# Kernel optimization log

Hardware: AMD Instinct MI355X
Metric: run time of the kernel (lower is better)

Reference implementation:

```python
import jax, jax.numpy as jnp
import numpy as np

N, E = 4096, 32768
NI, EI, D, EH = 64, 16, 64, 128
NUM_STEPS = 3


def setup_inputs() -> dict:
    key = jax.random.key(0)
    ks = jax.random.split(key, 24)

    def w(k, shape, fan_in):
        return (jax.random.normal(k, shape, jnp.float32) / np.float32(np.sqrt(fan_in)))

    return {
        "node_feats": jax.random.normal(ks[0], (N, NI), jnp.float32),
        "edge_attr": jax.random.normal(ks[1], (E, EI), jnp.float32),
        "edge_index": jax.random.randint(ks[2], (2, E), 0, N),
        # project_node_feats: Linear(NI -> D)
        "W_p": w(ks[3], (NI, D), NI), "b_p": jnp.zeros((D,), jnp.float32),
        # project_edge_feats: Linear(EI -> EH)
        "W_pe": w(ks[4], (EI, EH), EI), "b_pe": jnp.zeros((EH,), jnp.float32),
        # edge_network (NNConv nn): Linear(EH -> D*D)
        "W_nn": w(ks[5], (EH, D * D), EH), "b_nn": jnp.zeros((D * D,), jnp.float32),
        # NNConv root weight + bias
        "W_root": w(ks[6], (D, D), D), "b_conv": jnp.zeros((D,), jnp.float32),
        # GRU (single layer), gate order r, z, n as in torch
        "w_ih": w(ks[7], (D, 3 * D), D), "w_hh": w(ks[8], (D, 3 * D), D),
        "b_ih": jnp.zeros((3 * D,), jnp.float32), "b_hh": jnp.zeros((3 * D,), jnp.float32),
        # edge_update_network: Linear(EH+2D -> EH), Linear(EH -> EH)
        "W_eu1": w(ks[9], (EH + 2 * D, EH), EH + 2 * D), "b_eu1": jnp.zeros((EH,), jnp.float32),
        "W_eu2": w(ks[10], (EH, EH), EH), "b_eu2": jnp.zeros((EH,), jnp.float32),
    }


def reference(node_feats, edge_attr, edge_index, W_p, b_p, W_pe, b_pe,
              W_nn, b_nn, W_root, b_conv, w_ih, w_hh, b_ih, b_hh,
              W_eu1, b_eu1, W_eu2, b_eu2):
    relu = jax.nn.relu
    row, col = edge_index[0], edge_index[1]  # source, target
    n_nodes = node_feats.shape[0]
    d = W_root.shape[0]

    h = relu(node_feats @ W_p + b_p)          # (N, D) projected node feats
    hidden = h                                  # GRU hidden state
    e = relu(edge_attr @ W_pe + b_pe)          # (E, EH) projected edge feats

    for _ in range(NUM_STEPS):
        # NNConv: per-edge weight matrix from edge MLP (dropout=0 in eval)
        We = relu(e @ W_nn + b_nn).reshape(-1, d, d)      # (E, D, D)
        msg = jnp.einsum('ed,edf->ef', h[row], We)        # gather + per-edge matmul
        agg = jax.ops.segment_sum(msg, col, num_segments=n_nodes)  # scatter-add
        m = relu(agg + h @ W_root + b_conv)                # conv output + activation

        # GRU cell (torch gate order: r, z, n)
        gi = m @ w_ih + b_ih
        gh = hidden @ w_hh + b_hh
        ir, iz, i_n = jnp.split(gi, 3, axis=-1)
        hr, hz, h_n = jnp.split(gh, 3, axis=-1)
        r = jax.nn.sigmoid(ir + hr)
        z = jax.nn.sigmoid(iz + hz)
        ncand = jnp.tanh(i_n + r * h_n)
        hidden = (1.0 - z) * ncand + z * hidden
        h = hidden

        # edge update: cat(h[row], h[col], e) -> 2-layer MLP
        ei = jnp.concatenate([h[row], h[col], e], axis=1)
        e = relu(relu(ei @ W_eu1 + b_eu1) @ W_eu2 + b_eu2)

    return h, e
```

## Files before the change

### kernel.cpp

```cpp
#include <hip/hip_runtime.h>
#include <stdint.h>

typedef __attribute__((ext_vector_type(8))) _Float16 f16x8;
typedef __attribute__((ext_vector_type(4))) float f32x4;

#define N_NODES 4096
#define N_EDGES 32768

__device__ __forceinline__ float sigm(float x) { return 1.f / (1.f + __expf(-x)); }

__device__ __forceinline__ f16x8 packh8(const float* p) {
  f16x8 r;
#pragma unroll
  for (int i = 0; i < 8; ++i) r[i] = (_Float16)p[i];
  return r;
}

__device__ __forceinline__ void pinv(f16x8& x) { asm volatile("" : "+v"(x)); }

__global__ void zero_agg_kernel(float* __restrict__ agg) {
  agg[blockIdx.x * 256 + threadIdx.x] = 0.f;
}

__global__ void prep_all(const float* __restrict__ Wnn,
                         const float* __restrict__ We1,
                         const float* __restrict__ We2,
                         _Float16* __restrict__ WnnT,
                         _Float16* __restrict__ We1T,
                         _Float16* __restrict__ We2T) {
  __shared__ float tile[128][33];
  const int b = blockIdx.x, t = threadIdx.x;
  if (b < 128) {
    const int nb = b * 32;
    for (int i = 0; i < 16; ++i) {
      int g = i * 256 + t;
      int k = g >> 5, j = g & 31;
      tile[k][j] = Wnn[(size_t)k * 4096 + nb + j];
    }
    __syncthreads();
    for (int i = 0; i < 16; ++i) {
      int g = i * 256 + t;
      int j = g >> 7, k = g & 127;
      WnnT[(size_t)(nb + j) * 128 + k] = (_Float16)tile[k][j];
    }
  } else {
    int idx = (b - 128) * 256 + t;
    if (idx < 32768) {
      int n = idx >> 8, k = idx & 255;
      We1T[idx] = (_Float16)We1[(size_t)k * 128 + n];
    } else {
      int j = idx - 32768;
      int n = j >> 7, k = j & 127;
      We2T[j] = (_Float16)We2[(size_t)k * 128 + n];
    }
  }
}

__global__ void proj_node_f(const float* __restrict__ nf,
                            const float* __restrict__ Wp,
                            const float* __restrict__ bp,
                            float* __restrict__ h) {
  int idx = blockIdx.x * 256 + threadIdx.x;
  int n = idx >> 6, c = idx & 63;
  float acc = bp[c];
  for (int k = 0; k < 64; ++k)
    acc = fmaf(nf[n * 64 + k], Wp[k * 64 + c], acc);
  h[idx] = fmaxf(acc, 0.f);
}

__launch_bounds__(256)
__global__ void proj_edge_f2(const float* __restrict__ ea,
                             const float* __restrict__ Wpe,
                             const float* __restrict__ bpe,
                             float* __restrict__ e) {
  __shared__ float sw[16 * 128];
  __shared__ float sb[128];
  __shared__ float sa[32][17];
  const int t = threadIdx.x;
  const int ebase = blockIdx.x * 32;
  for (int g = t; g < 2048; g += 256) sw[g] = Wpe[g];
  if (t < 128) sb[t] = bpe[t];
  for (int g = t; g < 512; g += 256) {
    int r = g >> 4, k = g & 15;
    sa[r][k] = ea[(size_t)(ebase + r) * 16 + k];
  }
  __syncthreads();
  int c = t & 127, eg = t >> 7;
  float wc[16];
#pragma unroll
  for (int k = 0; k < 16; ++k) wc[k] = sw[k * 128 + c];
  float bv = sb[c];
#pragma unroll
  for (int i = 0; i < 16; ++i) {
    int ee = eg * 16 + i;
    float acc = bv;
#pragma unroll
    for (int k = 0; k < 16; ++k) acc = fmaf(sa[ee][k], wc[k], acc);
    e[(size_t)(ebase + ee) * 128 + c] = fmaxf(acc, 0.f);
  }
}

__launch_bounds__(512, 1)
__global__ void fused_msg_m(const float* __restrict__ ebf,
                            const float* __restrict__ hid,
                            const _Float16* __restrict__ WnnT,
                            const float* __restrict__ bnn,
                            const int* __restrict__ eidx,
                            float* __restrict__ agg) {
  __shared__ float Hs[64 * 132];
  const int t = threadIdx.x;
  const int w = t >> 6, l = t & 63, l15 = l & 15, q = l >> 4;
  const int fw = w & 3;
  const int eh = w >> 2;
  const int ebase = blockIdx.x * 128;

#pragma unroll
  for (int i = 0; i < 4; ++i) {
    int g = i * 512 + t;
    int e = g >> 4, d4 = g & 15;
    int r = eidx[ebase + e];
    float4 v = *(const float4*)&hid[(size_t)r * 64 + d4 * 4];
    Hs[(d4 * 4 + 0) * 132 + e] = v.x;
    Hs[(d4 * 4 + 1) * 132 + e] = v.y;
    Hs[(d4 * 4 + 2) * 132 + e] = v.z;
    Hs[(d4 * 4 + 3) * 132 + e] = v.w;
  }

  f16x8 af[4][4];
#pragma unroll
  for (int m = 0; m < 4; ++m)
#pragma unroll
    for (int kk = 0; kk < 4; ++kk) {
      af[m][kk] = packh8(&ebf[(size_t)(ebase + eh * 64 + m * 16 + l15) * 128 + kk * 32 + q * 8]);
      pinv(af[m][kk]);
    }

  float msg[4][4];
#pragma unroll
  for (int m = 0; m < 4; ++m)
#pragma unroll
    for (int rr = 0; rr < 4; ++rr) msg[m][rr] = 0.f;

  __syncthreads();

  const _Float16* wb = WnnT + (size_t)(fw * 16 + l15) * 128 + q * 8;
  f16x8 bb[4], nb[4];
#pragma unroll
  for (int kk = 0; kk < 4; ++kk) bb[kk] = *(const f16x8*)(wb + kk * 32);

  for (int d = 0; d < 64; ++d) {
    if (d < 63) {
      const _Float16* p = wb + (size_t)(d + 1) * 8192;
#pragma unroll
      for (int kk = 0; kk < 4; ++kk) nb[kk] = *(const f16x8*)(p + kk * 32);
    }
    float bnv = bnn[d * 64 + fw * 16 + l15];
#pragma unroll
    for (int m = 0; m < 4; ++m) {
      f32x4 C = {0.f, 0.f, 0.f, 0.f};
#pragma unroll
      for (int kk = 0; kk < 4; ++kk)
        C = __builtin_amdgcn_mfma_f32_16x16x32_f16(af[m][kk], bb[kk], C, 0, 0, 0);
      float4 hv = *(const float4*)&Hs[d * 132 + eh * 64 + m * 16 + q * 4];
      msg[m][0] = fmaf(hv.x, fmaxf(C[0] + bnv, 0.f), msg[m][0]);
      msg[m][1] = fmaf(hv.y, fmaxf(C[1] + bnv, 0.f), msg[m][1]);
      msg[m][2] = fmaf(hv.z, fmaxf(C[2] + bnv, 0.f), msg[m][2]);
      msg[m][3] = fmaf(hv.w, fmaxf(C[3] + bnv, 0.f), msg[m][3]);
    }
#pragma unroll
    for (int kk = 0; kk < 4; ++kk) bb[kk] = nb[kk];
  }

  const int* colp = eidx + N_EDGES;
#pragma unroll
  for (int m = 0; m < 4; ++m)
#pragma unroll
    for (int rr = 0; rr < 4; ++rr) {
      int col = colp[ebase + eh * 64 + m * 16 + q * 4 + rr];
      atomicAdd(&agg[(size_t)col * 64 + fw * 16 + l15], msg[m][rr]);
    }
}

__global__ void node_update_f(const float* __restrict__ agg_r,
                              float* __restrict__ agg_w,
                              float* __restrict__ hid,
                              const float* __restrict__ Wroot,
                              const float* __restrict__ bconv,
                              const float* __restrict__ wih,
                              const float* __restrict__ whh,
                              const float* __restrict__ bih,
                              const float* __restrict__ bhh) {
  __shared__ __align__(16) float sh[16 * 64];
  __shared__ __align__(16) float sm[16 * 64];
  __shared__ __align__(16) float sg[16 * 384];
  const int t = threadIdx.x;
  const int nb = blockIdx.x * 16;

  for (int i = 0; i < 4; ++i) sh[i * 256 + t] = hid[nb * 64 + i * 256 + t];
  __syncthreads();

  for (int i = 0; i < 4; ++i) {
    int idx = i * 256 + t;
    int nl = idx >> 6, dc = idx & 63;
    float acc = bconv[dc] + agg_r[nb * 64 + idx];
    for (int k = 0; k < 64; ++k)
      acc = fmaf(sh[nl * 64 + k], Wroot[k * 64 + dc], acc);
    sm[idx] = fmaxf(acc, 0.f);
  }
  __syncthreads();

  for (int i = 0; i < 24; ++i) {
    int idx = i * 256 + t;
    int nl = idx / 384, j2 = idx % 384;
    float acc;
    if (j2 < 192) {
      acc = bih[j2];
      for (int k = 0; k < 64; ++k)
        acc = fmaf(sm[nl * 64 + k], wih[k * 192 + j2], acc);
    } else {
      int j = j2 - 192;
      acc = bhh[j];
      for (int k = 0; k < 64; ++k)
        acc = fmaf(sh[nl * 64 + k], whh[k * 192 + j], acc);
    }
    sg[idx] = acc;
  }
  __syncthreads();

  for (int i = 0; i < 4; ++i) {
    int idx = i * 256 + t;
    int nl = idx >> 6, dc = idx & 63;
    const float* g = &sg[nl * 384];
    float ir = g[dc], iz = g[64 + dc], in_ = g[128 + dc];
    float hr = g[192 + dc], hz = g[256 + dc], hn = g[320 + dc];
    float r = sigm(ir + hr), z = sigm(iz + hz);
    float nc = tanhf(in_ + r * hn);
    hid[nb * 64 + idx] = (1.f - z) * nc + z * sh[nl * 64 + dc];
    agg_w[nb * 64 + idx] = 0.f;
  }
}

__launch_bounds__(256)
__global__ void edge_mlp_m(const float* __restrict__ hid,
                           float* __restrict__ ebf,
                           const int* __restrict__ eidx,
                           const _Float16* __restrict__ We1T,
                           const float* __restrict__ be1,
                           const _Float16* __restrict__ We2T,
                           const float* __restrict__ be2) {
  __shared__ _Float16 As[64 * 264];
  __shared__ _Float16 Ts[64 * 136];
  const int t = threadIdx.x;
  const int w = t >> 6, l = t & 63, l15 = l & 15, q = l >> 4;
  const int mbase = blockIdx.x * 64;

  for (int g = t; g < 2048; g += 256) {
    int r = g >> 5, kg = g & 31;
    int e = mbase + r;
    const float* src;
    if (kg < 8)       src = &hid[(size_t)eidx[e] * 64 + kg * 8];
    else if (kg < 16) src = &hid[(size_t)eidx[N_EDGES + e] * 64 + (kg - 8) * 8];
    else              src = &ebf[(size_t)e * 128 + (kg - 16) * 8];
    *(f16x8*)&As[r * 264 + kg * 8] = packh8(src);
  }
  __syncthreads();

  f32x4 zero4 = {0.f, 0.f, 0.f, 0.f};
  f32x4 acc[4][2];
#pragma unroll
  for (int m = 0; m < 4; ++m)
#pragma unroll
    for (int nn = 0; nn < 2; ++nn) acc[m][nn] = zero4;

#pragma unroll
  for (int kc = 0; kc < 4; ++kc)
#pragma unroll
    for (int kk = 0; kk < 2; ++kk) {
      int ko = kc * 64 + kk * 32 + q * 8;
      f16x8 b0 = *(const f16x8*)(We1T + (size_t)(w * 32 + l15) * 256 + ko);
      f16x8 b1 = *(const f16x8*)(We1T + (size_t)(w * 32 + 16 + l15) * 256 + ko);
#pragma unroll
      for (int m = 0; m < 4; ++m) {
        f16x8 a = *(const f16x8*)&As[(m * 16 + l15) * 264 + ko];
        acc[m][0] = __builtin_amdgcn_mfma_f32_16x16x32_f16(a, b0, acc[m][0], 0, 0, 0);
        acc[m][1] = __builtin_amdgcn_mfma_f32_16x16x32_f16(a, b1, acc[m][1], 0, 0, 0);
      }
    }

#pragma unroll
  for (int m = 0; m < 4; ++m)
#pragma unroll
    for (int nn = 0; nn < 2; ++nn) {
      int col = w * 32 + nn * 16 + l15;
      float bv = be1[col];
#pragma unroll
      for (int rr = 0; rr < 4; ++rr) {
        int row = m * 16 + q * 4 + rr;
        Ts[row * 136 + col] = (_Float16)fmaxf(acc[m][nn][rr] + bv, 0.f);
      }
    }
  __syncthreads();

  f32x4 acc2[4][2];
#pragma unroll
  for (int m = 0; m < 4; ++m)
#pragma unroll
    for (int nn = 0; nn < 2; ++nn) acc2[m][nn] = zero4;

#pragma unroll
  for (int kc = 0; kc < 2; ++kc)
#pragma unroll
    for (int kk = 0; kk < 2; ++kk) {
      int ko = kc * 64 + kk * 32 + q * 8;
      f16x8 b0 = *(const f16x8*)(We2T + (size_t)(w * 32 + l15) * 128 + ko);
      f16x8 b1 = *(const f16x8*)(We2T + (size_t)(w * 32 + 16 + l15) * 128 + ko);
#pragma unroll
      for (int m = 0; m < 4; ++m) {
        f16x8 a = *(const f16x8*)&Ts[(m * 16 + l15) * 136 + ko];
        acc2[m][0] = __builtin_amdgcn_mfma_f32_16x16x32_f16(a, b0, acc2[m][0], 0, 0, 0);
        acc2[m][1] = __builtin_amdgcn_mfma_f32_16x16x32_f16(a, b1, acc2[m][1], 0, 0, 0);
      }
    }

#pragma unroll
  for (int m = 0; m < 4; ++m)
#pragma unroll
    for (int nn = 0; nn < 2; ++nn) {
      int col = w * 32 + nn * 16 + l15;
      float bv = be2[col];
#pragma unroll
      for (int rr = 0; rr < 4; ++rr) {
        int row = mbase + m * 16 + q * 4 + rr;
        ebf[(size_t)row * 128 + col] = fmaxf(acc2[m][nn][rr] + bv, 0.f);
      }
    }
}

extern "C" void kernel_launch(void* const* d_in, const int* in_sizes, int n_in,
                              void* d_out, int out_size, void* d_ws, size_t ws_size,
                              hipStream_t stream) {
  const float* nf    = (const float*)d_in[0];
  const float* ea    = (const float*)d_in[1];
  const int*   eidx  = (const int*)d_in[2];
  const float* Wp    = (const float*)d_in[3];
  const float* bp    = (const float*)d_in[4];
  const float* Wpe   = (const float*)d_in[5];
  const float* bpe   = (const float*)d_in[6];
  const float* Wnn   = (const float*)d_in[7];
  const float* bnn   = (const float*)d_in[8];
  const float* Wroot = (const float*)d_in[9];
  const float* bconv = (const float*)d_in[10];
  const float* wih   = (const float*)d_in[11];
  const float* whh   = (const float*)d_in[12];
  const float* bih   = (const float*)d_in[13];
  const float* bhh   = (const float*)d_in[14];
  const float* We1   = (const float*)d_in[15];
  const float* be1   = (const float*)d_in[16];
  const float* We2   = (const float*)d_in[17];
  const float* be2   = (const float*)d_in[18];

  float* hid = (float*)d_out;
  float* ebf = (float*)d_out + 4096 * 64;

  char* ws = (char*)d_ws;
  _Float16* WnnT = (_Float16*)(ws + 0);
  _Float16* We1T = (_Float16*)(ws + 1048576);
  _Float16* We2T = (_Float16*)(ws + 1114112);
  float*    agg  = (float*)(ws + 1146880);

  prep_all<<<320, 256, 0, stream>>>(Wnn, We1, We2, WnnT, We1T, We2T);
  proj_node_f<<<1024, 256, 0, stream>>>(nf, Wp, bp, hid);
  proj_edge_f2<<<1024, 256, 0, stream>>>(ea, Wpe, bpe, ebf);
  zero_agg_kernel<<<1024, 256, 0, stream>>>(agg);

  for (int s = 0; s < 3; ++s) {
    fused_msg_m<<<256, 512, 0, stream>>>(ebf, hid, WnnT, bnn, eidx, agg);
    node_update_f<<<256, 256, 0, stream>>>(agg, agg, hid, Wroot, bconv,
                                           wih, whh, bih, bhh);
    edge_mlp_m<<<512, 256, 0, stream>>>(hid, ebf, eidx, We1T, be1, We2T, be2);
  }
}
```

Measured before the change: 545.7 us.

## Stage edge features in swizzled LDS and batch four d-slices per loop iteration

```diff
diff --git a/kernel.cpp b/kernel.cpp
--- a/kernel.cpp
+++ b/kernel.cpp
@@ -15,8 +15,6 @@
   for (int i = 0; i < 8; ++i) r[i] = (_Float16)p[i];
   return r;
 }
-
-__device__ __forceinline__ void pinv(f16x8& x) { asm volatile("" : "+v"(x)); }
 
 __global__ void zero_agg_kernel(float* __restrict__ agg) {
   agg[blockIdx.x * 256 + threadIdx.x] = 0.f;
@@ -107,7 +105,8 @@
                             const float* __restrict__ bnn,
                             const int* __restrict__ eidx,
                             float* __restrict__ agg) {
-  __shared__ float Hs[64 * 132];
+  __shared__ __align__(16) _Float16 Ae[128 * 128];
+  __shared__ __align__(16) float Hs[64 * 132];
   const int t = threadIdx.x;
   const int w = t >> 6, l = t & 63, l15 = l & 15, q = l >> 4;
   const int fw = w & 3;
@@ -125,15 +124,14 @@
     Hs[(d4 * 4 + 2) * 132 + e] = v.z;
     Hs[(d4 * 4 + 3) * 132 + e] = v.w;
   }
-
-  f16x8 af[4][4];
-#pragma unroll
-  for (int m = 0; m < 4; ++m)
-#pragma unroll
-    for (int kk = 0; kk < 4; ++kk) {
-      af[m][kk] = packh8(&ebf[(size_t)(ebase + eh * 64 + m * 16 + l15) * 128 + kk * 32 + q * 8]);
-      pinv(af[m][kk]);
-    }
+#pragma unroll
+  for (int i = 0; i < 4; ++i) {
+    int g = i * 512 + t;
+    int e = g >> 4, kg = g & 15;
+    f16x8 v = packh8(&ebf[(size_t)(ebase + e) * 128 + kg * 8]);
+    int kgp = kg ^ (e & 15);
+    *(f16x8*)&Ae[e * 128 + kgp * 8] = v;
+  }
 
   float msg[4][4];
 #pragma unroll
@@ -144,31 +142,45 @@
   __syncthreads();
 
   const _Float16* wb = WnnT + (size_t)(fw * 16 + l15) * 128 + q * 8;
-  f16x8 bb[4], nb[4];
-#pragma unroll
-  for (int kk = 0; kk < 4; ++kk) bb[kk] = *(const f16x8*)(wb + kk * 32);
-
-  for (int d = 0; d < 64; ++d) {
-    if (d < 63) {
-      const _Float16* p = wb + (size_t)(d + 1) * 8192;
-#pragma unroll
-      for (int kk = 0; kk < 4; ++kk) nb[kk] = *(const f16x8*)(p + kk * 32);
-    }
-    float bnv = bnn[d * 64 + fw * 16 + l15];
+
+#pragma unroll 1
+  for (int dg = 0; dg < 16; ++dg) {
+    f16x8 bb[4][4];
+#pragma unroll
+    for (int c = 0; c < 4; ++c) {
+      const _Float16* p = wb + (size_t)(dg * 4 + c) * 8192;
+#pragma unroll
+      for (int kk = 0; kk < 4; ++kk) bb[c][kk] = *(const f16x8*)(p + kk * 32);
+    }
+    float bnv[4];
+#pragma unroll
+    for (int c = 0; c < 4; ++c) bnv[c] = bnn[(dg * 4 + c) * 64 + fw * 16 + l15];
+
 #pragma unroll
     for (int m = 0; m < 4; ++m) {
-      f32x4 C = {0.f, 0.f, 0.f, 0.f};
-#pragma unroll
-      for (int kk = 0; kk < 4; ++kk)
-        C = __builtin_amdgcn_mfma_f32_16x16x32_f16(af[m][kk], bb[kk], C, 0, 0, 0);
-      float4 hv = *(const float4*)&Hs[d * 132 + eh * 64 + m * 16 + q * 4];
-      msg[m][0] = fmaf(hv.x, fmaxf(C[0] + bnv, 0.f), msg[m][0]);
-      msg[m][1] = fmaf(hv.y, fmaxf(C[1] + bnv, 0.f), msg[m][1]);
-      msg[m][2] = fmaf(hv.z, fmaxf(C[2] + bnv, 0.f), msg[m][2]);
-      msg[m][3] = fmaf(hv.w, fmaxf(C[3] + bnv, 0.f), msg[m][3]);
-    }
-#pragma unroll
-    for (int kk = 0; kk < 4; ++kk) bb[kk] = nb[kk];
+      const int arow = (eh * 64 + m * 16 + l15) * 128;
+      f32x4 C[4];
+#pragma unroll
+      for (int c = 0; c < 4; ++c) C[c] = (f32x4){0.f, 0.f, 0.f, 0.f};
+#pragma unroll
+      for (int kk = 0; kk < 4; ++kk) {
+        int kgp = (kk * 4 + q) ^ l15;
+        f16x8 a = *(const f16x8*)&Ae[arow + kgp * 8];
+#pragma unroll
+        for (int c = 0; c < 4; ++c)
+          C[c] = __builtin_amdgcn_mfma_f32_16x16x32_f16(a, bb[c][kk], C[c], 0, 0, 0);
+      }
+#pragma unroll
+      for (int c = 0; c < 4; ++c) {
+        int d = dg * 4 + c;
+        float4 hv = *(const float4*)&Hs[d * 132 + eh * 64 + m * 16 + q * 4];
+        msg[m][0] = fmaf(hv.x, fmaxf(C[c][0] + bnv[c], 0.f), msg[m][0]);
+        msg[m][1] = fmaf(hv.y, fmaxf(C[c][1] + bnv[c], 0.f), msg[m][1]);
+        msg[m][2] = fmaf(hv.z, fmaxf(C[c][2] + bnv[c], 0.f), msg[m][2]);
+        msg[m][3] = fmaf(hv.w, fmaxf(C[c][3] + bnv[c], 0.f), msg[m][3]);
+      }
+    }
+    asm volatile("" ::: "memory");
   }
 
   const int* colp = eidx + N_EDGES;
```

Result: faster. 504.4 us (-7.6%).
